# Kernel tuning notes

Measured on AMD Instinct MI355X. Metric: run time of the kernel, lower is better.

Reference implementation:

```python
import jax, jax.numpy as jnp
import numpy as np

B = 1048576
CARDS = np.array([2,2,2,2,2,3,3,4,4,4,4,4,4,5,5,5,5,5,5,5,2,2,2,2,2,2,2,2,2], dtype=np.int32)
NBR = 29  # number of categorical branches
EPS = 1e-5


def setup_inputs() -> dict:
    key = jax.random.key(0)
    ks = jax.random.split(key, 24)
    inp = {}
    inp['xcon'] = jax.random.normal(ks[0], (B, 7), dtype=jnp.float32)
    raw = jax.random.randint(ks[1], (B, NBR), 0, 5, dtype=jnp.int32)
    inp['xcat'] = raw % jnp.asarray(CARDS)[None, :]  # in-range per-branch indices
    s6 = 1.0 / np.sqrt(6.0)
    inp['emb_tables'] = jax.random.normal(ks[2], (NBR, 5, 6), dtype=jnp.float32)
    inp['w1'] = jax.random.normal(ks[3], (NBR, 6, 6), dtype=jnp.float32) * s6
    inp['b1'] = jax.random.normal(ks[4], (NBR, 6), dtype=jnp.float32) * s6
    inp['w2'] = jax.random.normal(ks[5], (NBR, 6), dtype=jnp.float32) * s6
    inp['b2'] = jax.random.normal(ks[6], (NBR,), dtype=jnp.float32) * s6
    inp['cbn_g'] = jnp.ones((7,), jnp.float32)
    inp['cbn_b'] = jnp.zeros((7,), jnp.float32)
    inp['cbn_m'] = jax.random.normal(ks[7], (7,), jnp.float32) * 0.1
    inp['cbn_v'] = jnp.ones((7,), jnp.float32) + 0.1 * jax.random.uniform(ks[8], (7,))
    dims = [(36, 36), (18, 36), (9, 18), (2, 9)]
    for i, (o, ic) in enumerate(dims, 1):
        s = 1.0 / np.sqrt(ic)
        inp[f'fc{i}_w'] = jax.random.normal(ks[8 + 2 * i], (o, ic), jnp.float32) * s
        inp[f'fc{i}_b'] = jax.random.normal(ks[9 + 2 * i], (o,), jnp.float32) * s
    for i, d in zip([1, 2, 3], [36, 18, 9]):
        inp[f'bn{i}_g'] = jnp.ones((d,), jnp.float32)
        inp[f'bn{i}_b'] = jnp.zeros((d,), jnp.float32)
        inp[f'bn{i}_m'] = jax.random.normal(jax.random.fold_in(key, 100 + i), (d,), jnp.float32) * 0.1
        inp[f'bn{i}_v'] = jnp.ones((d,), jnp.float32) + 0.1 * jax.random.uniform(jax.random.fold_in(key, 200 + i), (d,))
    return inp


def _bn(x, g, b, m, v):
    return (x - m) * jax.lax.rsqrt(v + EPS) * g + b


def reference(xcon, xcat, emb_tables, w1, b1, w2, b2,
              cbn_g, cbn_b, cbn_m, cbn_v,
              fc1_w, fc1_b, bn1_g, bn1_b, bn1_m, bn1_v,
              fc2_w, fc2_b, bn2_g, bn2_b, bn2_m, bn2_v,
              fc3_w, fc3_b, bn3_g, bn3_b, bn3_m, bn3_v,
              fc4_w, fc4_b):
    # Batched gather over all 29 branches: [B,29,6]
    emb = emb_tables[jnp.arange(NBR)[None, :], xcat]
    # Per-branch tiny MLP, fused as batched GEMMs
    h = jax.nn.relu(jnp.einsum('bjd,jde->bje', emb, w1) + b1)   # [B,29,6]
    xcatemb = jnp.einsum('bjd,jd->bj', h, w2) + b2              # [B,29]
    # (catdo_layer dropout is identity in eval mode)
    xcon_n = _bn(xcon, cbn_g, cbn_b, cbn_m, cbn_v)              # BatchNorm1d(7), eval
    xin = jnp.concatenate([xcon_n, xcatemb], axis=1)            # [B,36]
    h1 = jax.nn.relu(_bn(xin @ fc1_w.T + fc1_b, bn1_g, bn1_b, bn1_m, bn1_v))
    h2 = jax.nn.relu(_bn(h1 @ fc2_w.T + fc2_b, bn2_g, bn2_b, bn2_m, bn2_v))
    h3 = jax.nn.relu(_bn(h2 @ fc3_w.T + fc3_b, bn3_g, bn3_b, bn3_m, bn3_v))
    logits = h3 @ fc4_w.T + fc4_b                               # [B,2]
    return jax.nn.softmax(logits, axis=1)
```

## Files before the change

### kernel.cpp

```cpp
#include <hip/hip_runtime.h>

typedef _Float16 f16x8 __attribute__((ext_vector_type(8)));
typedef __fp16 fp16x2 __attribute__((ext_vector_type(2)));
typedef float f32x4 __attribute__((ext_vector_type(4)));

#define NTHR 256
constexpr int NBR = 29;
constexpr float EPS = 1e-5f;
constexpr int NBLOCKS = 4096;

#define TAB_B   0
#define W1_B    1024
#define W2_B    7168
#define W3_B    11264
#define B1_B    12288
#define B2_B    12544
#define B3_B    12672
#define W4_B    12736
#define B4_B    12800

__device__ __forceinline__ ushort f16bits(float x) {
    union { _Float16 h; ushort u; } c; c.h = (_Float16)x; return c.u;
}

__device__ __forceinline__ uint pk2(float a, float b) {
    union { fp16x2 h; uint u; } c; c.h = __builtin_amdgcn_cvt_pkrtz(a, b); return c.u;
}

__device__ __forceinline__ f16x8 lda_frag(const char* xb, int row, int kb, int g) {
    int base = row * 128 + kb * 2 + 8 * g;
    int sw = (row & 7) << 4;
    uint2 lo = *(const uint2*)(xb + (base ^ sw));
    uint2 hi = *(const uint2*)(xb + ((base + 32) ^ sw));
    union { uint u[4]; f16x8 v; } f;
    f.u[0] = lo.x; f.u[1] = lo.y; f.u[2] = hi.x; f.u[3] = hi.y;
    return f.v;
}

__device__ __forceinline__ f16x8 ldb_frag(const ushort* wp, int n, int stride, int kb, int g) {
    const ushort* p = wp + n * stride + kb + 4 * g;
    uint2 lo = *(const uint2*)p;
    uint2 hi = *(const uint2*)(p + 16);
    union { uint u[4]; f16x8 v; } f;
    f.u[0] = lo.x; f.u[1] = lo.y; f.u[2] = hi.x; f.u[3] = hi.y;
    return f.v;
}

__global__ __launch_bounds__(NTHR) void prep_kernel(
    const float* __restrict__ embt, const float* __restrict__ w1,
    const float* __restrict__ b1,   const float* __restrict__ w2,
    const float* __restrict__ b2,
    const float* __restrict__ cbn_g, const float* __restrict__ cbn_b,
    const float* __restrict__ cbn_m, const float* __restrict__ cbn_v,
    const float* __restrict__ f1w, const float* __restrict__ f1b,
    const float* __restrict__ f2w, const float* __restrict__ f2b,
    const float* __restrict__ f3w, const float* __restrict__ f3b,
    const float* __restrict__ f4w, const float* __restrict__ f4b,
    const float* __restrict__ bn1g, const float* __restrict__ bn1b,
    const float* __restrict__ bn1m, const float* __restrict__ bn1v,
    const float* __restrict__ bn2g, const float* __restrict__ bn2b,
    const float* __restrict__ bn2m, const float* __restrict__ bn2v,
    const float* __restrict__ bn3g, const float* __restrict__ bn3b,
    const float* __restrict__ bn3m, const float* __restrict__ bn3v,
    char* __restrict__ ws)
{
    const int t = threadIdx.x;
    float* tab = (float*)(ws + TAB_B);
    ushort* w1o = (ushort*)(ws + W1_B);
    ushort* w2o = (ushort*)(ws + W2_B);
    ushort* w3o = (ushort*)(ws + W3_B);
    float* b1o = (float*)(ws + B1_B);
    float* b2o = (float*)(ws + B2_B);
    float* b3o = (float*)(ws + B3_B);
    float* w4o = (float*)(ws + W4_B);
    float* b4o = (float*)(ws + B4_B);

    for (int i = t; i < 232; i += NTHR) {
        int j = i / 8, c = i % 8;
        float xe = 0.f;
        if (c < 5) {
            xe = b2[j];
            for (int e = 0; e < 6; e++) {
                float a = b1[j * 6 + e];
                for (int d = 0; d < 6; d++)
                    a += embt[(j * 5 + c) * 6 + d] * w1[j * 36 + d * 6 + e];
                xe += fmaxf(a, 0.f) * w2[j * 6 + e];
            }
        }
        tab[i] = xe;
    }
    for (int i = t; i < 3072; i += NTHR) {
        int n = i / 64, k = i % 64;
        float v = 0.f;
        if (n < 36 && k < 36) {
            float s1 = bn1g[n] * rsqrtf(bn1v[n] + EPS);
            v = f1w[n * 36 + k] * s1;
            if (k < 7) v *= cbn_g[k] * rsqrtf(cbn_v[k] + EPS);
        }
        w1o[i] = f16bits(v);
    }
    if (t < 48) {
        float v = 0.f;
        if (t < 36) {
            float s1 = bn1g[t] * rsqrtf(bn1v[t] + EPS);
            v = f1b[t] * s1 + bn1b[t] - bn1m[t] * s1;
            for (int k = 0; k < 7; k++) {
                float cs = cbn_g[k] * rsqrtf(cbn_v[k] + EPS);
                float ct = cbn_b[k] - cbn_m[k] * cs;
                v += f1w[t * 36 + k] * s1 * ct;
            }
        }
        b1o[t] = v;
    }
    for (int i = t; i < 2048; i += NTHR) {
        int n = i / 64, k = i % 64;
        float v = 0.f;
        if (n < 18 && k < 36) {
            float s = bn2g[n] * rsqrtf(bn2v[n] + EPS);
            v = f2w[n * 36 + k] * s;
        }
        w2o[i] = f16bits(v);
    }
    if (t < 32) {
        float v = 0.f;
        if (t < 18) {
            float s = bn2g[t] * rsqrtf(bn2v[t] + EPS);
            v = f2b[t] * s + bn2b[t] - bn2m[t] * s;
        }
        b2o[t] = v;
    }
    for (int i = t; i < 512; i += NTHR) {
        int n = i / 32, k = i % 32;
        float v = 0.f;
        if (n < 9 && k < 18) {
            float s = bn3g[n] * rsqrtf(bn3v[n] + EPS);
            v = f3w[n * 18 + k] * s;
        }
        w3o[i] = f16bits(v);
    }
    if (t < 16) {
        float v = 0.f;
        if (t < 9) {
            float s = bn3g[t] * rsqrtf(bn3v[t] + EPS);
            v = f3b[t] * s + bn3b[t] - bn3m[t] * s;
        }
        b3o[t] = v;
    }
    if (t < 16) w4o[t] = (t < 9) ? (f4w[9 + t] - f4w[t]) : 0.f;
    if (t == 0) b4o[0] = f4b[1] - f4b[0];
}

__global__ __launch_bounds__(NTHR, 3) void recovery_net_kernel(
    const float* __restrict__ xcon, const int* __restrict__ xcat,
    const char* __restrict__ ws, float2* __restrict__ out)
{
    __shared__ ushort s_x[16384];
    __shared__ uint  s_catp[1856];
    __shared__ float s_xcon[1792];
    __shared__ float s_tab[928];

    const int t = threadIdx.x;
    const int lane = t & 63, w = t >> 6;
    const int l15 = lane & 15, g = lane >> 4;
    char* xb = (char*)s_x;

    {
        const int4* src = (const int4*)(xcat + (size_t)blockIdx.x * 7424);
        for (int i = t; i < 1856; i += NTHR) {
            int4 v = src[i];
            s_catp[i] = (uint)(v.x & 0xff) | ((uint)(v.y & 0xff) << 8) |
                        ((uint)(v.z & 0xff) << 16) | ((uint)(v.w & 0xff) << 24);
        }
        const float4* s2 = (const float4*)(xcon + (size_t)blockIdx.x * 1792);
        for (int i = t; i < 448; i += NTHR) ((float4*)s_xcon)[i] = s2[i];
        const float* tws = (const float*)(ws + TAB_B);
        for (int cp = 0; cp < 4; cp++)
            for (int i = t; i < 232; i += NTHR) s_tab[cp * 232 + i] = tws[i];
    }
    __syncthreads();

    {
        const unsigned char* myc = ((const unsigned char*)s_catp) + t * 29;
        const float* tb = s_tab + ((t >> 4) & 3) * 232;
        float v[64];
#pragma unroll
        for (int k = 0; k < 7; k++) v[k] = s_xcon[t * 7 + k];
#pragma unroll
        for (int j = 0; j < 29; j++) v[7 + j] = tb[j * 8 + (int)myc[j]];
#pragma unroll
        for (int k = 36; k < 64; k++) v[k] = 0.f;
        const int rbase = t * 128, sw = (t & 7) << 4;
#pragma unroll
        for (int j = 0; j < 8; j++) {
            uint p0 = pk2(v[8 * j + 0], v[8 * j + 1]);
            uint p1 = pk2(v[8 * j + 2], v[8 * j + 3]);
            uint p2 = pk2(v[8 * j + 4], v[8 * j + 5]);
            uint p3 = pk2(v[8 * j + 6], v[8 * j + 7]);
            *(uint4*)(xb + ((rbase + j * 16) ^ sw)) = make_uint4(p0, p1, p2, p3);
        }
    }

    const int rb = w * 64;
    const ushort* w1p = (const ushort*)(ws + W1_B);
    const ushort* w2p = (const ushort*)(ws + W2_B);
    const ushort* w3p = (const ushort*)(ws + W3_B);
    const float* b1p = (const float*)(ws + B1_B);
    const float* b2p = (const float*)(ws + B2_B);
    const float* b3p = (const float*)(ws + B3_B);
    const float* w4p = (const float*)(ws + W4_B);
    const float* b4p = (const float*)(ws + B4_B);

    {
        f16x8 bf[3][2];
#pragma unroll
        for (int nt = 0; nt < 3; nt++) {
            bf[nt][0] = ldb_frag(w1p, nt * 16 + l15, 64, 0, g);
            bf[nt][1] = ldb_frag(w1p, nt * 16 + l15, 64, 32, g);
        }
        f32x4 acc[4][3];
#pragma unroll
        for (int nt = 0; nt < 3; nt++) {
            float bv = b1p[nt * 16 + l15];
#pragma unroll
            for (int mt = 0; mt < 4; mt++) acc[mt][nt] = f32x4{bv, bv, bv, bv};
        }
#pragma unroll
        for (int mt = 0; mt < 4; mt++) {
            f16x8 a0 = lda_frag(xb, rb + mt * 16 + l15, 0, g);
            f16x8 a1 = lda_frag(xb, rb + mt * 16 + l15, 32, g);
#pragma unroll
            for (int nt = 0; nt < 3; nt++) {
                acc[mt][nt] = __builtin_amdgcn_mfma_f32_16x16x32_f16(a0, bf[nt][0], acc[mt][nt], 0, 0, 0);
                acc[mt][nt] = __builtin_amdgcn_mfma_f32_16x16x32_f16(a1, bf[nt][1], acc[mt][nt], 0, 0, 0);
            }
        }
#pragma unroll
        for (int mt = 0; mt < 4; mt++)
#pragma unroll
            for (int nt = 0; nt < 3; nt++)
#pragma unroll
                for (int r = 0; r < 4; r++) {
                    int row = rb + mt * 16 + 4 * g + r;
                    int col = nt * 16 + l15;
                    int b = (row * 128 + col * 2) ^ ((row & 7) << 4);
                    *(ushort*)(xb + b) = f16bits(fmaxf(acc[mt][nt][r], 0.f));
                }
    }

    {
        f16x8 bf[2][2];
#pragma unroll
        for (int nt = 0; nt < 2; nt++) {
            bf[nt][0] = ldb_frag(w2p, nt * 16 + l15, 64, 0, g);
            bf[nt][1] = ldb_frag(w2p, nt * 16 + l15, 64, 32, g);
        }
        f32x4 acc[4][2];
#pragma unroll
        for (int nt = 0; nt < 2; nt++) {
            float bv = b2p[nt * 16 + l15];
#pragma unroll
            for (int mt = 0; mt < 4; mt++) acc[mt][nt] = f32x4{bv, bv, bv, bv};
        }
#pragma unroll
        for (int mt = 0; mt < 4; mt++) {
            f16x8 a0 = lda_frag(xb, rb + mt * 16 + l15, 0, g);
            f16x8 a1 = lda_frag(xb, rb + mt * 16 + l15, 32, g);
#pragma unroll
            for (int nt = 0; nt < 2; nt++) {
                acc[mt][nt] = __builtin_amdgcn_mfma_f32_16x16x32_f16(a0, bf[nt][0], acc[mt][nt], 0, 0, 0);
                acc[mt][nt] = __builtin_amdgcn_mfma_f32_16x16x32_f16(a1, bf[nt][1], acc[mt][nt], 0, 0, 0);
            }
        }
#pragma unroll
        for (int mt = 0; mt < 4; mt++)
#pragma unroll
            for (int nt = 0; nt < 2; nt++)
#pragma unroll
                for (int r = 0; r < 4; r++) {
                    int row = rb + mt * 16 + 4 * g + r;
                    int col = nt * 16 + l15;
                    int b = (row * 128 + col * 2) ^ ((row & 7) << 4);
                    *(ushort*)(xb + b) = f16bits(fmaxf(acc[mt][nt][r], 0.f));
                }
    }

    {
        f16x8 bf = ldb_frag(w3p, l15, 32, 0, g);
        float bv = b3p[l15];
        float w4v = w4p[l15];
        float b4v = *b4p;
        f32x4 acc[4];
#pragma unroll
        for (int mt = 0; mt < 4; mt++) acc[mt] = f32x4{bv, bv, bv, bv};
#pragma unroll
        for (int mt = 0; mt < 4; mt++) {
            f16x8 a0 = lda_frag(xb, rb + mt * 16 + l15, 0, g);
            acc[mt] = __builtin_amdgcn_mfma_f32_16x16x32_f16(a0, bf, acc[mt], 0, 0, 0);
        }
#pragma unroll
        for (int mt = 0; mt < 4; mt++) {
            float dr[4];
#pragma unroll
            for (int r = 0; r < 4; r++) {
                float x = fmaxf(acc[mt][r], 0.f) * w4v;
                x += __shfl_xor(x, 1);
                x += __shfl_xor(x, 2);
                x += __shfl_xor(x, 4);
                x += __shfl_xor(x, 8);
                dr[r] = x;
            }
            float d = (l15 == 0) ? dr[0] : (l15 == 1) ? dr[1] : (l15 == 2) ? dr[2] : dr[3];
            d += b4v;
            float p1 = 1.f / (1.f + __expf(-d));
            if (l15 < 4) {
                int row = blockIdx.x * 256 + rb + mt * 16 + 4 * g + l15;
                out[row] = make_float2(1.f - p1, p1);
            }
        }
    }
}

extern "C" void kernel_launch(void* const* d_in, const int* in_sizes, int n_in,
                              void* d_out, int out_size, void* d_ws, size_t ws_size,
                              hipStream_t stream) {
    (void)in_sizes; (void)n_in; (void)ws_size; (void)out_size;
    char* ws = (char*)d_ws;
    prep_kernel<<<1, NTHR, 0, stream>>>(
        (const float*)d_in[2],  (const float*)d_in[3],
        (const float*)d_in[4],  (const float*)d_in[5],
        (const float*)d_in[6],
        (const float*)d_in[7],  (const float*)d_in[8],
        (const float*)d_in[9],  (const float*)d_in[10],
        (const float*)d_in[11], (const float*)d_in[12],
        (const float*)d_in[13], (const float*)d_in[14],
        (const float*)d_in[15], (const float*)d_in[16],
        (const float*)d_in[17], (const float*)d_in[18],
        (const float*)d_in[19], (const float*)d_in[20],
        (const float*)d_in[21], (const float*)d_in[22],
        (const float*)d_in[23], (const float*)d_in[24],
        (const float*)d_in[25], (const float*)d_in[26],
        (const float*)d_in[27], (const float*)d_in[28],
        (const float*)d_in[29], (const float*)d_in[30],
        ws);
    recovery_net_kernel<<<NBLOCKS, NTHR, 0, stream>>>(
        (const float*)d_in[0], (const int*)d_in[1], ws, (float2*)d_out);
}
```

Before: 84.43 us.

## Chain MLP layers in registers via transposed MFMA, shrink shared-memory staging

The three MFMA layers now run in transposed form, with the weights as the A operand and the activations as B. Each layer's accumulator output is packed straight into the next layer's B fragment in registers, so the intermediate activations no longer round-trip through shared memory. The input staging buffer shrinks to an 88-byte row stride holding only 36 halves, the table copies are cut from 4 to 2, and the launch bounds go to 4 blocks per CU to raise occupancy. The final reduction now uses two cross-group shuffles instead of four. The risk is the register pressure of keeping every weight fragment resident, plus possible LDS bank conflicts from the new unswizzled stride.

```diff
diff --git a/kernel.cpp b/kernel.cpp
--- a/kernel.cpp
+++ b/kernel.cpp
@@ -5,7 +5,6 @@
 typedef float f32x4 __attribute__((ext_vector_type(4)));
 
 #define NTHR 256
-constexpr int NBR = 29;
 constexpr float EPS = 1e-5f;
 constexpr int NBLOCKS = 4096;
 
@@ -22,28 +21,23 @@
 __device__ __forceinline__ ushort f16bits(float x) {
     union { _Float16 h; ushort u; } c; c.h = (_Float16)x; return c.u;
 }
-
 __device__ __forceinline__ uint pk2(float a, float b) {
     union { fp16x2 h; uint u; } c; c.h = __builtin_amdgcn_cvt_pkrtz(a, b); return c.u;
 }
-
-__device__ __forceinline__ f16x8 lda_frag(const char* xb, int row, int kb, int g) {
-    int base = row * 128 + kb * 2 + 8 * g;
-    int sw = (row & 7) << 4;
-    uint2 lo = *(const uint2*)(xb + (base ^ sw));
-    uint2 hi = *(const uint2*)(xb + ((base + 32) ^ sw));
+__device__ __forceinline__ uint pkrelu(float a, float b) {
+    return pk2(fmaxf(a, 0.f), fmaxf(b, 0.f));
+}
+__device__ __forceinline__ f16x8 mk8(uint a, uint b, uint c, uint d) {
     union { uint u[4]; f16x8 v; } f;
-    f.u[0] = lo.x; f.u[1] = lo.y; f.u[2] = hi.x; f.u[3] = hi.y;
+    f.u[0] = a; f.u[1] = b; f.u[2] = c; f.u[3] = d;
     return f.v;
 }
 
-__device__ __forceinline__ f16x8 ldb_frag(const ushort* wp, int n, int stride, int kb, int g) {
-    const ushort* p = wp + n * stride + kb + 4 * g;
+__device__ __forceinline__ f16x8 ldw_frag(const ushort* wp, int m, int stride, int kb, int g) {
+    const ushort* p = wp + m * stride + kb + 4 * g;
     uint2 lo = *(const uint2*)p;
     uint2 hi = *(const uint2*)(p + 16);
-    union { uint u[4]; f16x8 v; } f;
-    f.u[0] = lo.x; f.u[1] = lo.y; f.u[2] = hi.x; f.u[3] = hi.y;
-    return f.v;
+    return mk8(lo.x, lo.y, hi.x, hi.y);
 }
 
 __global__ __launch_bounds__(NTHR) void prep_kernel(
@@ -150,19 +144,20 @@
     if (t == 0) b4o[0] = f4b[1] - f4b[0];
 }
 
-__global__ __launch_bounds__(NTHR, 3) void recovery_net_kernel(
+#define XSTRIDE 88
+
+__global__ __launch_bounds__(NTHR, 4) void recovery_net_kernel(
     const float* __restrict__ xcon, const int* __restrict__ xcat,
     const char* __restrict__ ws, float2* __restrict__ out)
 {
-    __shared__ ushort s_x[16384];
+    __shared__ __align__(16) char s_x[256 * XSTRIDE];
     __shared__ uint  s_catp[1856];
     __shared__ float s_xcon[1792];
-    __shared__ float s_tab[928];
+    __shared__ float s_tab[464];
 
     const int t = threadIdx.x;
     const int lane = t & 63, w = t >> 6;
     const int l15 = lane & 15, g = lane >> 4;
-    char* xb = (char*)s_x;
 
     {
         const int4* src = (const int4*)(xcat + (size_t)blockIdx.x * 7424);
@@ -174,30 +169,25 @@
         const float4* s2 = (const float4*)(xcon + (size_t)blockIdx.x * 1792);
         for (int i = t; i < 448; i += NTHR) ((float4*)s_xcon)[i] = s2[i];
         const float* tws = (const float*)(ws + TAB_B);
-        for (int cp = 0; cp < 4; cp++)
-            for (int i = t; i < 232; i += NTHR) s_tab[cp * 232 + i] = tws[i];
+        for (int i = t; i < 464; i += NTHR) s_tab[i] = tws[i % 232];
     }
     __syncthreads();
 
     {
         const unsigned char* myc = ((const unsigned char*)s_catp) + t * 29;
-        const float* tb = s_tab + ((t >> 4) & 3) * 232;
-        float v[64];
+        const float* tb = s_tab + ((t >> 5) & 1) * 232;
+        float v[36];
 #pragma unroll
         for (int k = 0; k < 7; k++) v[k] = s_xcon[t * 7 + k];
 #pragma unroll
         for (int j = 0; j < 29; j++) v[7 + j] = tb[j * 8 + (int)myc[j]];
-#pragma unroll
-        for (int k = 36; k < 64; k++) v[k] = 0.f;
-        const int rbase = t * 128, sw = (t & 7) << 4;
-#pragma unroll
-        for (int j = 0; j < 8; j++) {
-            uint p0 = pk2(v[8 * j + 0], v[8 * j + 1]);
-            uint p1 = pk2(v[8 * j + 2], v[8 * j + 3]);
-            uint p2 = pk2(v[8 * j + 4], v[8 * j + 5]);
-            uint p3 = pk2(v[8 * j + 6], v[8 * j + 7]);
-            *(uint4*)(xb + ((rbase + j * 16) ^ sw)) = make_uint4(p0, p1, p2, p3);
-        }
+        uint wd[18];
+#pragma unroll
+        for (int j = 0; j < 18; j++) wd[j] = pk2(v[2 * j], v[2 * j + 1]);
+        char* xb = s_x + t * XSTRIDE;
+#pragma unroll
+        for (int j = 0; j < 9; j++)
+            *(uint2*)(xb + 8 * j) = make_uint2(wd[2 * j], wd[2 * j + 1]);
     }
 
     const int rb = w * 64;
@@ -210,113 +200,71 @@
     const float* w4p = (const float*)(ws + W4_B);
     const float* b4p = (const float*)(ws + B4_B);
 
-    {
-        f16x8 bf[3][2];
-#pragma unroll
-        for (int nt = 0; nt < 3; nt++) {
-            bf[nt][0] = ldb_frag(w1p, nt * 16 + l15, 64, 0, g);
-            bf[nt][1] = ldb_frag(w1p, nt * 16 + l15, 64, 32, g);
-        }
-        f32x4 acc[4][3];
-#pragma unroll
-        for (int nt = 0; nt < 3; nt++) {
-            float bv = b1p[nt * 16 + l15];
-#pragma unroll
-            for (int mt = 0; mt < 4; mt++) acc[mt][nt] = f32x4{bv, bv, bv, bv};
-        }
-#pragma unroll
-        for (int mt = 0; mt < 4; mt++) {
-            f16x8 a0 = lda_frag(xb, rb + mt * 16 + l15, 0, g);
-            f16x8 a1 = lda_frag(xb, rb + mt * 16 + l15, 32, g);
-#pragma unroll
-            for (int nt = 0; nt < 3; nt++) {
-                acc[mt][nt] = __builtin_amdgcn_mfma_f32_16x16x32_f16(a0, bf[nt][0], acc[mt][nt], 0, 0, 0);
-                acc[mt][nt] = __builtin_amdgcn_mfma_f32_16x16x32_f16(a1, bf[nt][1], acc[mt][nt], 0, 0, 0);
-            }
-        }
-#pragma unroll
-        for (int mt = 0; mt < 4; mt++)
-#pragma unroll
-            for (int nt = 0; nt < 3; nt++)
-#pragma unroll
-                for (int r = 0; r < 4; r++) {
-                    int row = rb + mt * 16 + 4 * g + r;
-                    int col = nt * 16 + l15;
-                    int b = (row * 128 + col * 2) ^ ((row & 7) << 4);
-                    *(ushort*)(xb + b) = f16bits(fmaxf(acc[mt][nt][r], 0.f));
-                }
-    }
-
-    {
-        f16x8 bf[2][2];
-#pragma unroll
-        for (int nt = 0; nt < 2; nt++) {
-            bf[nt][0] = ldb_frag(w2p, nt * 16 + l15, 64, 0, g);
-            bf[nt][1] = ldb_frag(w2p, nt * 16 + l15, 64, 32, g);
-        }
-        f32x4 acc[4][2];
-#pragma unroll
-        for (int nt = 0; nt < 2; nt++) {
-            float bv = b2p[nt * 16 + l15];
-#pragma unroll
-            for (int mt = 0; mt < 4; mt++) acc[mt][nt] = f32x4{bv, bv, bv, bv};
-        }
-#pragma unroll
-        for (int mt = 0; mt < 4; mt++) {
-            f16x8 a0 = lda_frag(xb, rb + mt * 16 + l15, 0, g);
-            f16x8 a1 = lda_frag(xb, rb + mt * 16 + l15, 32, g);
-#pragma unroll
-            for (int nt = 0; nt < 2; nt++) {
-                acc[mt][nt] = __builtin_amdgcn_mfma_f32_16x16x32_f16(a0, bf[nt][0], acc[mt][nt], 0, 0, 0);
-                acc[mt][nt] = __builtin_amdgcn_mfma_f32_16x16x32_f16(a1, bf[nt][1], acc[mt][nt], 0, 0, 0);
-            }
-        }
-#pragma unroll
-        for (int mt = 0; mt < 4; mt++)
-#pragma unroll
-            for (int nt = 0; nt < 2; nt++)
-#pragma unroll
-                for (int r = 0; r < 4; r++) {
-                    int row = rb + mt * 16 + 4 * g + r;
-                    int col = nt * 16 + l15;
-                    int b = (row * 128 + col * 2) ^ ((row & 7) << 4);
-                    *(ushort*)(xb + b) = f16bits(fmaxf(acc[mt][nt][r], 0.f));
-                }
-    }
-
-    {
-        f16x8 bf = ldb_frag(w3p, l15, 32, 0, g);
-        float bv = b3p[l15];
-        float w4v = w4p[l15];
-        float b4v = *b4p;
-        f32x4 acc[4];
-#pragma unroll
-        for (int mt = 0; mt < 4; mt++) acc[mt] = f32x4{bv, bv, bv, bv};
-#pragma unroll
-        for (int mt = 0; mt < 4; mt++) {
-            f16x8 a0 = lda_frag(xb, rb + mt * 16 + l15, 0, g);
-            acc[mt] = __builtin_amdgcn_mfma_f32_16x16x32_f16(a0, bf, acc[mt], 0, 0, 0);
-        }
-#pragma unroll
-        for (int mt = 0; mt < 4; mt++) {
-            float dr[4];
-#pragma unroll
-            for (int r = 0; r < 4; r++) {
-                float x = fmaxf(acc[mt][r], 0.f) * w4v;
-                x += __shfl_xor(x, 1);
-                x += __shfl_xor(x, 2);
-                x += __shfl_xor(x, 4);
-                x += __shfl_xor(x, 8);
-                dr[r] = x;
-            }
-            float d = (l15 == 0) ? dr[0] : (l15 == 1) ? dr[1] : (l15 == 2) ? dr[2] : dr[3];
-            d += b4v;
-            float p1 = 1.f / (1.f + __expf(-d));
-            if (l15 < 4) {
-                int row = blockIdx.x * 256 + rb + mt * 16 + 4 * g + l15;
-                out[row] = make_float2(1.f - p1, p1);
-            }
-        }
+    f16x8 a1[3][2], a2[2][2], a3;
+#pragma unroll
+    for (int mt = 0; mt < 3; mt++) {
+        a1[mt][0] = ldw_frag(w1p, mt * 16 + l15, 64, 0, g);
+        a1[mt][1] = ldw_frag(w1p, mt * 16 + l15, 64, 32, g);
+    }
+#pragma unroll
+    for (int mt = 0; mt < 2; mt++) {
+        a2[mt][0] = ldw_frag(w2p, mt * 16 + l15, 64, 0, g);
+        a2[mt][1] = ldw_frag(w2p, mt * 16 + l15, 64, 32, g);
+    }
+    a3 = ldw_frag(w3p, l15, 32, 0, g);
+
+    const float4 b1v0 = *(const float4*)(b1p + 4 * g);
+    const float4 b1v1 = *(const float4*)(b1p + 16 + 4 * g);
+    const float4 b1v2 = *(const float4*)(b1p + 32 + 4 * g);
+    const float4 b2v0 = *(const float4*)(b2p + 4 * g);
+    const float4 b2v1 = *(const float4*)(b2p + 16 + 4 * g);
+    const float4 b3v  = *(const float4*)(b3p + 4 * g);
+    const float4 w4v  = *(const float4*)(w4p + 4 * g);
+    const float b4s = *b4p;
+
+#pragma unroll
+    for (int bt = 0; bt < 4; bt++) {
+        const char* xr = s_x + (rb + 16 * bt + l15) * XSTRIDE;
+        uint2 q0 = *(const uint2*)(xr + 8 * g);
+        uint2 q1 = *(const uint2*)(xr + 32 + 8 * g);
+        uint2 q2 = *(const uint2*)(xr + 64);
+        f16x8 xb0 = mk8(q0.x, q0.y, q1.x, q1.y);
+        f16x8 xb1 = mk8(g == 0 ? q2.x : 0u, g == 0 ? q2.y : 0u, 0u, 0u);
+
+        f32x4 c10 = f32x4{b1v0.x, b1v0.y, b1v0.z, b1v0.w};
+        f32x4 c11 = f32x4{b1v1.x, b1v1.y, b1v1.z, b1v1.w};
+        f32x4 c12 = f32x4{b1v2.x, b1v2.y, b1v2.z, b1v2.w};
+        c10 = __builtin_amdgcn_mfma_f32_16x16x32_f16(a1[0][0], xb0, c10, 0, 0, 0);
+        c11 = __builtin_amdgcn_mfma_f32_16x16x32_f16(a1[1][0], xb0, c11, 0, 0, 0);
+        c12 = __builtin_amdgcn_mfma_f32_16x16x32_f16(a1[2][0], xb0, c12, 0, 0, 0);
+        c10 = __builtin_amdgcn_mfma_f32_16x16x32_f16(a1[0][1], xb1, c10, 0, 0, 0);
+        c11 = __builtin_amdgcn_mfma_f32_16x16x32_f16(a1[1][1], xb1, c11, 0, 0, 0);
+        c12 = __builtin_amdgcn_mfma_f32_16x16x32_f16(a1[2][1], xb1, c12, 0, 0, 0);
+
+        f16x8 h0 = mk8(pkrelu(c10.x, c10.y), pkrelu(c10.z, c10.w),
+                       pkrelu(c11.x, c11.y), pkrelu(c11.z, c11.w));
+        f16x8 h1 = mk8(pkrelu(c12.x, c12.y), pkrelu(c12.z, c12.w), 0u, 0u);
+
+        f32x4 c20 = f32x4{b2v0.x, b2v0.y, b2v0.z, b2v0.w};
+        f32x4 c21 = f32x4{b2v1.x, b2v1.y, b2v1.z, b2v1.w};
+        c20 = __builtin_amdgcn_mfma_f32_16x16x32_f16(a2[0][0], h0, c20, 0, 0, 0);
+        c21 = __builtin_amdgcn_mfma_f32_16x16x32_f16(a2[1][0], h0, c21, 0, 0, 0);
+        c20 = __builtin_amdgcn_mfma_f32_16x16x32_f16(a2[0][1], h1, c20, 0, 0, 0);
+        c21 = __builtin_amdgcn_mfma_f32_16x16x32_f16(a2[1][1], h1, c21, 0, 0, 0);
+
+        f16x8 h2 = mk8(pkrelu(c20.x, c20.y), pkrelu(c20.z, c20.w),
+                       pkrelu(c21.x, c21.y), pkrelu(c21.z, c21.w));
+        f32x4 c3 = f32x4{b3v.x, b3v.y, b3v.z, b3v.w};
+        c3 = __builtin_amdgcn_mfma_f32_16x16x32_f16(a3, h2, c3, 0, 0, 0);
+
+        float part = fmaxf(c3.x, 0.f) * w4v.x + fmaxf(c3.y, 0.f) * w4v.y +
+                     fmaxf(c3.z, 0.f) * w4v.z + fmaxf(c3.w, 0.f) * w4v.w;
+        part += __shfl_xor(part, 16);
+        part += __shfl_xor(part, 32);
+        float d = part + b4s;
+        float p1 = 1.f / (1.f + __expf(-d));
+        if (g == 0)
+            out[blockIdx.x * 256 + rb + 16 * bt + l15] = make_float2(1.f - p1, p1);
     }
 }
 
```

New measurement: 77.92 us. 7.7% less time.
